# Performance work log

Measured on AMD Instinct MI355X. Metric: run time of the kernel, lower is better.

The kernel has to match this reference:

```python
import jax, jax.numpy as jnp
import numpy as np

B, S, C, L = 8, 256, 4, 256
E, H, NL, NS = 256, 8, 2, 8
DH = E // H
EPS = 1e-5


def _conv1d(x, w, b):
    # x: [B, Cin, L], w: [Cout, Cin, K] -> [B, Cout, L] (SAME padding, stride 1)
    y = jax.lax.conv_general_dilated(x, w, (1,), 'SAME', dimension_numbers=('NCH', 'OIH', 'NCH'))
    return y + b[None, :, None]


def _local_cnn(xs, w1, b1, w2, b2):
    # xs: [B, 4, L] for one segment; per-segment weights
    h = jax.nn.relu(_conv1d(xs, w1, b1))
    h = jax.nn.relu(_conv1d(h, w2, b2))
    return jnp.max(h, axis=-1)  # AdaptiveMaxPool1d(1) + squeeze -> [B, E]


def _layernorm(x, g, b):
    m = jnp.mean(x, axis=-1, keepdims=True)
    v = jnp.mean((x - m) ** 2, axis=-1, keepdims=True)
    return (x - m) / jnp.sqrt(v + EPS) * g + b


def setup_inputs() -> dict:
    key = jax.random.key(0)
    ks = jax.random.split(key, 24)
    n = lambda k, shp, s: jax.random.normal(k, shp, jnp.float32) * s
    return {
        'x': jax.random.normal(ks[0], (B, S, C, L), jnp.float32),
        'conv1_w': n(ks[1], (S, 128, 4, 3), 0.1), 'conv1_b': jnp.zeros((S, 128), jnp.float32),
        'conv2_w': n(ks[2], (S, E, 128, 3), 0.05), 'conv2_b': jnp.zeros((S, E), jnp.float32),
        'ln1_g': jnp.ones((NL, E), jnp.float32), 'ln1_b': jnp.zeros((NL, E), jnp.float32),
        'wq': n(ks[3], (NL, E, E), 0.02), 'bq': jnp.zeros((NL, E), jnp.float32),
        'wk': n(ks[4], (NL, E, E), 0.02), 'bk': jnp.zeros((NL, E), jnp.float32),
        'wv': n(ks[5], (NL, E, E), 0.02), 'bv': jnp.zeros((NL, E), jnp.float32),
        'wo': n(ks[6], (NL, E, E), 0.02), 'bo': jnp.zeros((NL, E), jnp.float32),
        'bias_w': n(ks[7], (NL, 4, H), 0.1), 'bias_b': jnp.zeros((NL, H), jnp.float32),
        'ln2_g': jnp.ones((NL, E), jnp.float32), 'ln2_b': jnp.zeros((NL, E), jnp.float32),
        'ffn_w1': n(ks[8], (NL, E, 2 * E), 0.02), 'ffn_b1': jnp.zeros((NL, 2 * E), jnp.float32),
        'ffn_w2': n(ks[9], (NL, 2 * E, E), 0.02), 'ffn_b2': jnp.zeros((NL, E), jnp.float32),
        'fc_w': n(ks[10], (NS * E, 2), 0.02), 'fc_b': jnp.zeros((2,), jnp.float32),
    }


def _forward(x, conv1_w, conv1_b, conv2_w, conv2_b, ln1_g, ln1_b,
             wq, bq, wk, bk, wv, bv, wo, bo, bias_w, bias_b,
             ln2_g, ln2_b, ffn_w1, ffn_b1, ffn_w2, ffn_b2, fc_w, fc_b):
    # Per-segment CNNs (vmap over segment axis with per-segment weights) -> [B, S, E]
    cnn = jax.vmap(_local_cnn, in_axes=(1, 0, 0, 0, 0), out_axes=1)(x, conv1_w, conv1_b, conv2_w, conv2_b)
    feat = _layernorm(cnn, jnp.ones((E,), cnn.dtype), jnp.zeros((E,), cnn.dtype))  # F.layer_norm, no affine

    # bias matrices: cdist (p=2), global-max normalized; positional distance; inverses
    sq = jnp.sum(feat * feat, axis=-1)  # [B, S]
    d2 = sq[:, :, None] + sq[:, None, :] - 2.0 * jnp.einsum('bie,bje->bij', feat, feat)
    dist = jnp.sqrt(jnp.maximum(d2, 0.0))
    dist = dist / (jnp.max(dist) + 1e-6)
    idx = jnp.arange(S, dtype=feat.dtype)
    rdist = jnp.abs(idx[:, None] - idx[None, :]) / (S - 1)
    rdist = jnp.broadcast_to(rdist[None], (feat.shape[0], S, S))
    attn_bias = jnp.stack([dist, rdist, 1.0 - rdist, 1.0 - dist], axis=-1)  # [B,S,S,4]

    h = feat
    scale = 1.0 / jnp.sqrt(jnp.asarray(DH, h.dtype))
    for l in range(NL):
        hn = _layernorm(h, ln1_g[l], ln1_b[l])
        q = (hn @ wq[l] + bq[l]).reshape(-1, S, H, DH)
        k = (hn @ wk[l] + bk[l]).reshape(-1, S, H, DH)
        v = (hn @ wv[l] + bv[l]).reshape(-1, S, H, DH)
        scores = jnp.einsum('bihd,bjhd->bhij', q, k) * scale
        scores = scores + jnp.einsum('bijc,ch->bhij', attn_bias, bias_w[l]) + bias_b[l][None, :, None, None]
        a = jax.nn.softmax(scores, axis=-1)
        o = jnp.einsum('bhij,bjhd->bihd', a, v).reshape(-1, S, E) @ wo[l] + bo[l]
        h = h + o
        hn2 = _layernorm(h, ln2_g[l], ln2_b[l])
        f = jax.nn.relu(hn2 @ ffn_w1[l] + ffn_b1[l]) @ ffn_w2[l] + ffn_b2[l]
        h = h + f

    # split into NS chunks along segments, max-pool each, concat (S % NS == 0)
    pooled = jnp.max(h.reshape(-1, NS, S // NS, E), axis=2).reshape(-1, NS * E)
    return pooled @ fc_w + fc_b  # [B, num_classes]


def reference(x, conv1_w, conv1_b, conv2_w, conv2_b, ln1_g, ln1_b,
              wq, bq, wk, bk, wv, bv, wo, bo, bias_w, bias_b,
              ln2_g, ln2_b, ffn_w1, ffn_b1, ffn_w2, ffn_b2, fc_w, fc_b):
    return _forward(x, conv1_w, conv1_b, conv2_w, conv2_b, ln1_g, ln1_b,
                    wq, bq, wk, bk, wv, bv, wo, bo, bias_w, bias_b,
                    ln2_g, ln2_b, ffn_w1, ffn_b1, ffn_w2, ffn_b2, fc_w, fc_b)
```

## Files before the change

kernel.cpp:

```cpp
#include <hip/hip_runtime.h>
#include <hip/hip_bf16.h>


typedef float floatx4 __attribute__((ext_vector_type(4)));
typedef short bf16x8 __attribute__((ext_vector_type(8)));

__device__ __forceinline__ float wave_sum(float v) {
    v += __shfl_xor(v, 32); v += __shfl_xor(v, 16); v += __shfl_xor(v, 8);
    v += __shfl_xor(v, 4);  v += __shfl_xor(v, 2);  v += __shfl_xor(v, 1);
    return v;
}
__device__ __forceinline__ float wave_max(float v) {
    v = fmaxf(v, __shfl_xor(v, 32)); v = fmaxf(v, __shfl_xor(v, 16));
    v = fmaxf(v, __shfl_xor(v, 8));  v = fmaxf(v, __shfl_xor(v, 4));
    v = fmaxf(v, __shfl_xor(v, 2));  v = fmaxf(v, __shfl_xor(v, 1));
    return v;
}
__device__ __forceinline__ unsigned short f2bf(float v) {
    unsigned b = __float_as_uint(v);
    unsigned r = (b + 0x7fffu + ((b >> 16) & 1u)) >> 16;
    return (unsigned short)r;
}

__global__ void init_kernel(unsigned* dmax, unsigned* cnnmax) {
    const size_t i = (size_t)blockIdx.x * 256 + threadIdx.x;
    cnnmax[i] = 0u;
    if (i == 0) *dmax = 0u;
}

__global__ __launch_bounds__(256) void prep_w2_kernel(
    const float* __restrict__ w2, unsigned short* __restrict__ w2b)
{
    const int s = blockIdx.x;
    const int part = blockIdx.y;
    const float* src = w2 + (size_t)s * 98304;
    unsigned short* dst = w2b + (size_t)s * 98304;
    for (int o = part * 24576 + threadIdx.x; o < (part + 1) * 24576; o += 256) {
        const int kk = o % 384, co = o / 384;
        const int ci = kk & 127, tap = kk >> 7;
        dst[o] = f2bf(src[(size_t)co * 384 + ci * 3 + tap]);
    }
}

__global__ __launch_bounds__(512) void conv2_fused_kernel(
    const unsigned short* __restrict__ w2b,
    const float* __restrict__ x,
    const float* __restrict__ w1,
    const float* __restrict__ b1,
    const float* __restrict__ b2,
    unsigned* __restrict__ cnnmax)
{
    __shared__ float xs[4][258];
    __shared__ float w1s[1536];
    __shared__ unsigned short Hs[130 * 136];
    const int tid = threadIdx.x;
    const int lane = tid & 63;
    const int wv = __builtin_amdgcn_readfirstlane((int)(tid >> 6));
    const int wm = wv & 3, wn = wv >> 2;
    const int s = blockIdx.x;
    const int nt = blockIdx.y;
    const int b = nt >> 1;
    const int l0 = (nt & 1) * 128;
    const int lr = lane & 15;
    const int quad = lane >> 4;
    const int qk = quad * 8;

    const float* xp = x + ((size_t)(b * 256 + s)) * 1024;
    for (int i = tid; i < 1024; i += 512) {
        const int ci = i >> 8, l = i & 255;
        xs[ci][l + 1] = xp[i];
    }
    if (tid < 4) { xs[tid][0] = 0.f; xs[tid][257] = 0.f; }
    const float* w1p = w1 + (size_t)s * 1536;
    for (int i = tid; i < 1536; i += 512) w1s[i] = w1p[i];
    __syncthreads();

    {
        const int co = tid & 127;
        const int g = tid >> 7;
        float wreg[12];
#pragma unroll
        for (int k = 0; k < 12; k++) wreg[k] = w1s[co * 12 + k];
        const float bb1 = b1[s * 128 + co];
        for (int pr = g; pr < 130; pr += 4) {
            const int l = l0 - 1 + pr;
            float a = 0.f;
            if ((unsigned)l < 256u) {
                a = bb1;
#pragma unroll
                for (int ci = 0; ci < 4; ci++)
#pragma unroll
                    for (int k = 0; k < 3; k++) a = fmaf(wreg[ci * 3 + k], xs[ci][l + k], a);
                a = fmaxf(a, 0.f);
            }
            Hs[pr * 136 + co] = f2bf(a);
        }
    }
    __syncthreads();

    floatx4 acc[4][4];
#pragma unroll
    for (int r = 0; r < 4; r++)
#pragma unroll
        for (int c = 0; c < 4; c++) acc[r][c] = (floatx4){0.f, 0.f, 0.f, 0.f};

    const int co_base = wm * 64;
    const unsigned short* wp = w2b + ((size_t)(s * 256 + co_base + lr)) * 384 + qk;
    const int nb = wn * 64;

#pragma unroll
    for (int tap = 0; tap < 3; tap++) {
#pragma unroll
        for (int ci0 = 0; ci0 < 128; ci0 += 32) {
            const int kk0 = tap * 128 + ci0;
            bf16x8 a[4], bb[4];
#pragma unroll
            for (int r = 0; r < 4; r++)
                a[r] = *(const bf16x8*)(wp + r * (16 * 384) + kk0);
#pragma unroll
            for (int c = 0; c < 4; c++) {
                const int rl = nb + c * 16 + lr + tap;
                bb[c] = *(const bf16x8*)(&Hs[rl * 136 + ci0 + qk]);
            }
#pragma unroll
            for (int r = 0; r < 4; r++)
#pragma unroll
                for (int c = 0; c < 4; c++)
                    acc[r][c] = __builtin_amdgcn_mfma_f32_16x16x32_bf16(a[r], bb[c], acc[r][c], 0, 0, 0);
        }
    }

    const float* b2s = b2 + s * 256;
    unsigned* cmrow = cnnmax + ((size_t)(b * 256 + s)) * 256;
#pragma unroll
    for (int r = 0; r < 4; r++) {
#pragma unroll
        for (int e = 0; e < 4; e++) {
            const int co = co_base + r * 16 + quad * 4 + e;
            const float bias = b2s[co];
            float mv = 0.f;
#pragma unroll
            for (int c = 0; c < 4; c++) mv = fmaxf(mv, acc[r][c][e] + bias);
            mv = fmaxf(mv, __shfl_xor(mv, 1));
            mv = fmaxf(mv, __shfl_xor(mv, 2));
            mv = fmaxf(mv, __shfl_xor(mv, 4));
            mv = fmaxf(mv, __shfl_xor(mv, 8));
            if (lr == 0) atomicMax(&cmrow[co], __float_as_uint(mv));
        }
    }
}

__global__ __launch_bounds__(256) void ln0_kernel(
    const unsigned* __restrict__ cm, float* __restrict__ out, float* __restrict__ sqv)
{
    const int tid = threadIdx.x, lane = tid & 63, wid = tid >> 6;
    const int row = blockIdx.x * 4 + wid;
    const unsigned* xr = cm + (size_t)row * 256;
    float v[4];
#pragma unroll
    for (int i = 0; i < 4; i++) v[i] = __uint_as_float(xr[lane + 64 * i]);
    float sm = wave_sum(v[0] + v[1] + v[2] + v[3]);
    const float mean = sm * (1.f / 256.f);
    float qv = 0.f;
#pragma unroll
    for (int i = 0; i < 4; i++) { const float d = v[i] - mean; qv = fmaf(d, d, qv); }
    qv = wave_sum(qv);
    const float inv = rsqrtf(qv * (1.f / 256.f) + 1e-5f);
    float* orow = out + (size_t)row * 256;
#pragma unroll
    for (int i = 0; i < 4; i++) orow[lane + 64 * i] = (v[i] - mean) * inv;
    if (lane == 0) sqv[row] = qv * inv * inv;
}

__global__ __launch_bounds__(256) void dist_kernel(
    const float* __restrict__ feat, const float* __restrict__ sq,
    float* __restrict__ dist, unsigned* __restrict__ dmax)
{
    __shared__ float Fi[32][260];
    __shared__ float Fj[16][260];
    __shared__ float redm[4];
    const int tid = threadIdx.x;
    const int bid = blockIdx.x;
    const int b = bid >> 7, it = (bid >> 4) & 7, jt = bid & 15;
    const float* fb = feat + (size_t)b * 65536;
    for (int idx = tid; idx < 32 * 256; idx += 256) {
        const int r = idx >> 8, e = idx & 255;
        Fi[r][e] = fb[(it * 32 + r) * 256 + e];
    }
    for (int idx = tid; idx < 16 * 256; idx += 256) {
        const int r = idx >> 8, e = idx & 255;
        Fj[r][e] = fb[(jt * 16 + r) * 256 + e];
    }
    __syncthreads();
    const int ii = tid >> 3, j0 = (tid & 7) * 2;
    float acc[2] = {0.f, 0.f};
    for (int e = 0; e < 256; e += 4) {
        const float4 a = *(const float4*)&Fi[ii][e];
#pragma unroll
        for (int u = 0; u < 2; u++) {
            const float4 bv = *(const float4*)&Fj[j0 + u][e];
            acc[u] += a.x * bv.x + a.y * bv.y + a.z * bv.z + a.w * bv.w;
        }
    }
    const float sqi = sq[b * 256 + it * 32 + ii];
    float mymax = 0.f;
#pragma unroll
    for (int u = 0; u < 2; u++) {
        const float d2 = sqi + sq[b * 256 + jt * 16 + j0 + u] - 2.f * acc[u];
        const float d = sqrtf(fmaxf(d2, 0.f));
        dist[((size_t)b * 256 + it * 32 + ii) * 256 + jt * 16 + j0 + u] = d;
        mymax = fmaxf(mymax, d);
    }
    mymax = wave_max(mymax);
    if ((tid & 63) == 0) redm[tid >> 6] = mymax;
    __syncthreads();
    if (tid == 0) {
        const float m = fmaxf(fmaxf(redm[0], redm[1]), fmaxf(redm[2], redm[3]));
        atomicMax(dmax, __float_as_uint(m));
    }
}

__global__ __launch_bounds__(256) void ln_bf_kernel(
    const float* __restrict__ x, const float* __restrict__ g, const float* __restrict__ bta,
    unsigned short* __restrict__ out)
{
    const int tid = threadIdx.x, lane = tid & 63, wid = tid >> 6;
    const int row = blockIdx.x * 4 + wid;
    const float* xr = x + (size_t)row * 256;
    float v[4];
#pragma unroll
    for (int i = 0; i < 4; i++) v[i] = xr[lane + 64 * i];
    float sm = wave_sum(v[0] + v[1] + v[2] + v[3]);
    const float mean = sm * (1.f / 256.f);
    float q = 0.f;
#pragma unroll
    for (int i = 0; i < 4; i++) { const float d = v[i] - mean; q = fmaf(d, d, q); }
    q = wave_sum(q);
    const float inv = rsqrtf(q * (1.f / 256.f) + 1e-5f);
    unsigned short* orow = out + (size_t)row * 256;
#pragma unroll
    for (int i = 0; i < 4; i++) {
        const int e = lane + 64 * i;
        orow[e] = f2bf((v[i] - mean) * inv * g[e] + bta[e]);
    }
}

__global__ __launch_bounds__(256) void prep_wt_kernel(
    const float* __restrict__ wq, const float* __restrict__ wk, const float* __restrict__ wv,
    const float* __restrict__ wo, const float* __restrict__ f1, const float* __restrict__ f2,
    unsigned short* __restrict__ wtb)
{
    __shared__ float t[32][33];
    const int z = blockIdx.z;
    const int l = z / 6, id = z % 6;
    const float* src; int K_, N_; size_t doff;
    switch (id) {
        case 0:  src = wq + (size_t)l * 65536;  K_ = 256; N_ = 256; doff = 0;      break;
        case 1:  src = wk + (size_t)l * 65536;  K_ = 256; N_ = 256; doff = 65536;  break;
        case 2:  src = wv + (size_t)l * 65536;  K_ = 256; N_ = 256; doff = 131072; break;
        case 3:  src = wo + (size_t)l * 65536;  K_ = 256; N_ = 256; doff = 196608; break;
        case 4:  src = f1 + (size_t)l * 131072; K_ = 256; N_ = 512; doff = 262144; break;
        default: src = f2 + (size_t)l * 131072; K_ = 512; N_ = 256; doff = 393216; break;
    }
    const int k0 = blockIdx.x * 32, n0 = blockIdx.y * 32;
    if (k0 >= K_ || n0 >= N_) return;
    unsigned short* dst = wtb + (size_t)l * 524288 + doff;
    const int c = threadIdx.x & 31, rq = threadIdx.x >> 5;
#pragma unroll
    for (int i = 0; i < 4; i++) {
        const int r = rq + i * 8;
        t[r][c] = src[(size_t)(k0 + r) * N_ + n0 + c];
    }
    __syncthreads();
#pragma unroll
    for (int i = 0; i < 4; i++) {
        const int r = rq + i * 8;
        dst[(size_t)(n0 + r) * K_ + k0 + c] = f2bf(t[c][r]);
    }
}

__global__ __launch_bounds__(128) void gemm_mfma_kernel(
    const unsigned short* __restrict__ A, const unsigned short* __restrict__ Wt,
    const float* __restrict__ b0, const float* __restrict__ b1, const float* __restrict__ b2,
    const float* __restrict__ R, float* __restrict__ outf,
    unsigned short* __restrict__ o0, unsigned short* __restrict__ o1, unsigned short* __restrict__ o2,
    int K, int mode)
{
    const int tid = threadIdx.x;
    const int lane = tid & 63, lr = lane & 15, quad = lane >> 4;
    const int wv = __builtin_amdgcn_readfirstlane((int)(tid >> 6));
    const int m0 = blockIdx.x * 128 + wv * 64;
    const int n0 = blockIdx.y * 32;

    floatx4 acc[4][2];
#pragma unroll
    for (int r = 0; r < 4; r++)
#pragma unroll
        for (int c = 0; c < 2; c++) acc[r][c] = (floatx4){0.f, 0.f, 0.f, 0.f};

    const unsigned short* Ap = A + (size_t)(m0 + lr) * K + quad * 8;
    const unsigned short* Bp = Wt + (size_t)(n0 + lr) * K + quad * 8;
    const int nks = K >> 5;
#pragma unroll 4
    for (int ks = 0; ks < nks; ks++) {
        const int ko = ks * 32;
        bf16x8 a[4], b[2];
#pragma unroll
        for (int r = 0; r < 4; r++) a[r] = *(const bf16x8*)(Ap + (size_t)r * 16 * K + ko);
#pragma unroll
        for (int c = 0; c < 2; c++) b[c] = *(const bf16x8*)(Bp + (size_t)c * 16 * K + ko);
#pragma unroll
        for (int r = 0; r < 4; r++)
#pragma unroll
            for (int c = 0; c < 2; c++)
                acc[r][c] = __builtin_amdgcn_mfma_f32_16x16x32_bf16(a[r], b[c], acc[r][c], 0, 0, 0);
    }

    if (mode == 0) {
        const int which = n0 >> 8, nn0 = n0 & 255;
        if (which < 2) {
            unsigned short* op = which ? o1 : o0;
            const float* bp = which ? b1 : b0;
#pragma unroll
            for (int r = 0; r < 4; r++)
#pragma unroll
                for (int c = 0; c < 2; c++)
#pragma unroll
                    for (int e = 0; e < 4; e++) {
                        const int m = m0 + r * 16 + quad * 4 + e;
                        const int n = nn0 + c * 16 + lr;
                        op[(size_t)m * 256 + n] = f2bf(acc[r][c][e] + bp[n]);
                    }
        } else {
#pragma unroll
            for (int r = 0; r < 4; r++)
#pragma unroll
                for (int c = 0; c < 2; c++)
#pragma unroll
                    for (int e = 0; e < 4; e++) {
                        const int m = m0 + r * 16 + quad * 4 + e;
                        const int nn = nn0 + c * 16 + lr;
                        const int bb_ = m >> 8, j = m & 255, hh = nn >> 5, d = nn & 31;
                        o2[(size_t)((bb_ * 8 + hh) * 32 + d) * 256 + j] = f2bf(acc[r][c][e] + b2[nn]);
                    }
        }
    } else if (mode == 1) {
#pragma unroll
        for (int r = 0; r < 4; r++)
#pragma unroll
            for (int c = 0; c < 2; c++)
#pragma unroll
                for (int e = 0; e < 4; e++) {
                    const int m = m0 + r * 16 + quad * 4 + e;
                    const int n = n0 + c * 16 + lr;
                    outf[(size_t)m * 256 + n] = acc[r][c][e] + b0[n] + R[(size_t)m * 256 + n];
                }
    } else {
#pragma unroll
        for (int r = 0; r < 4; r++)
#pragma unroll
            for (int c = 0; c < 2; c++)
#pragma unroll
                for (int e = 0; e < 4; e++) {
                    const int m = m0 + r * 16 + quad * 4 + e;
                    const int n = n0 + c * 16 + lr;
                    o0[(size_t)m * 512 + n] = f2bf(fmaxf(acc[r][c][e] + b0[n], 0.f));
                }
    }
}

__global__ __launch_bounds__(256) void attn_mfma_kernel(
    const unsigned short* __restrict__ q_bf, const unsigned short* __restrict__ k_bf,
    const unsigned short* __restrict__ vt_bf,
    const float* __restrict__ dist, const unsigned* __restrict__ dmax,
    const float* __restrict__ bw, const float* __restrict__ bb,
    unsigned short* __restrict__ ao_bf)
{
    __shared__ unsigned short Ps[4][16][264];
    const int tid = threadIdx.x;
    const int lane = tid & 63, lr = lane & 15, quad = lane >> 4;
    const int wv = __builtin_amdgcn_readfirstlane((int)(tid >> 6));
    const int ic = blockIdx.x, hh = blockIdx.y, b = blockIdx.z;
    const int i0 = ic * 64 + wv * 16;

    const float dinv = 1.f / (__uint_as_float(*dmax) + 1e-6f);
    const float w0 = bw[0 * 8 + hh], w1 = bw[1 * 8 + hh], w2 = bw[2 * 8 + hh], w3 = bw[3 * 8 + hh];
    const float bbh = bb[hh];
    const float scale = 0.17677669529663687f;

    const bf16x8 aq = *(const bf16x8*)(q_bf + (size_t)(b * 256 + i0 + lr) * 256 + hh * 32 + quad * 8);
    floatx4 sc[16];
#pragma unroll
    for (int c = 0; c < 16; c++) {
        const bf16x8 bk = *(const bf16x8*)(k_bf + (size_t)(b * 256 + c * 16 + lr) * 256 + hh * 32 + quad * 8);
        sc[c] = __builtin_amdgcn_mfma_f32_16x16x32_bf16(aq, bk, (floatx4){0.f, 0.f, 0.f, 0.f}, 0, 0, 0);
    }

#pragma unroll
    for (int e = 0; e < 4; e++) {
        const int i = i0 + quad * 4 + e;
        const float* drow = dist + ((size_t)(b * 256 + i)) * 256;
        float bs[16];
        float mx = -1e30f;
#pragma unroll
        for (int c = 0; c < 16; c++) {
            const int j = c * 16 + lr;
            const float dn = drow[j] * dinv;
            const float rd = fabsf((float)(i - j)) * (1.f / 255.f);
            bs[c] = sc[c][e] * scale + w0 * dn + w1 * rd + w2 * (1.f - rd) + w3 * (1.f - dn) + bbh;
            mx = fmaxf(mx, bs[c]);
        }
        mx = fmaxf(mx, __shfl_xor(mx, 1)); mx = fmaxf(mx, __shfl_xor(mx, 2));
        mx = fmaxf(mx, __shfl_xor(mx, 4)); mx = fmaxf(mx, __shfl_xor(mx, 8));
        float sm = 0.f;
#pragma unroll
        for (int c = 0; c < 16; c++) { bs[c] = __expf(bs[c] - mx); sm += bs[c]; }
        sm += __shfl_xor(sm, 1); sm += __shfl_xor(sm, 2);
        sm += __shfl_xor(sm, 4); sm += __shfl_xor(sm, 8);
        const float rs = 1.f / sm;
#pragma unroll
        for (int c = 0; c < 16; c++)
            Ps[wv][quad * 4 + e][c * 16 + lr] = f2bf(bs[c] * rs);
    }
    __syncthreads();

    floatx4 oc[2];
    oc[0] = (floatx4){0.f, 0.f, 0.f, 0.f};
    oc[1] = (floatx4){0.f, 0.f, 0.f, 0.f};
    const unsigned short* vtb = vt_bf + (size_t)(b * 8 + hh) * 8192;
#pragma unroll
    for (int ks = 0; ks < 8; ks++) {
        const bf16x8 ap = *(const bf16x8*)(&Ps[wv][lr][ks * 32 + quad * 8]);
#pragma unroll
        for (int c2 = 0; c2 < 2; c2++) {
            const bf16x8 bvv = *(const bf16x8*)(vtb + (size_t)(c2 * 16 + lr) * 256 + ks * 32 + quad * 8);
            oc[c2] = __builtin_amdgcn_mfma_f32_16x16x32_bf16(ap, bvv, oc[c2], 0, 0, 0);
        }
    }
#pragma unroll
    for (int c2 = 0; c2 < 2; c2++)
#pragma unroll
        for (int e = 0; e < 4; e++)
            ao_bf[(size_t)(b * 256 + i0 + quad * 4 + e) * 256 + hh * 32 + c2 * 16 + lr] = f2bf(oc[c2][e]);
}

__global__ __launch_bounds__(256) void pool_fc_kernel(
    const float* __restrict__ h, const float* __restrict__ fcw,
    const float* __restrict__ fcb, float* __restrict__ out)
{
    __shared__ float red[8];
    const int b = blockIdx.x, tid = threadIdx.x, lane = tid & 63, wid = tid >> 6;
    float a0 = 0.f, a1 = 0.f;
    for (int ns = 0; ns < 8; ns++) {
        const float* hp = h + ((size_t)(b * 256 + ns * 32)) * 256 + tid;
        float m = hp[0];
#pragma unroll
        for (int r = 1; r < 32; r++) m = fmaxf(m, hp[(size_t)r * 256]);
        a0 = fmaf(m, fcw[(ns * 256 + tid) * 2 + 0], a0);
        a1 = fmaf(m, fcw[(ns * 256 + tid) * 2 + 1], a1);
    }
    a0 = wave_sum(a0);
    a1 = wave_sum(a1);
    if (lane == 0) { red[wid] = a0; red[4 + wid] = a1; }
    __syncthreads();
    if (tid == 0) out[b * 2 + 0] = red[0] + red[1] + red[2] + red[3] + fcb[0];
    if (tid == 1) out[b * 2 + 1] = red[4] + red[5] + red[6] + red[7] + fcb[1];
}

extern "C" void kernel_launch(void* const* d_in, const int* in_sizes, int n_in,
                              void* d_out, int out_size, void* d_ws, size_t ws_size,
                              hipStream_t stream)
{
    (void)in_sizes; (void)n_in; (void)out_size; (void)ws_size;
    const float* x       = (const float*)d_in[0];
    const float* conv1_w = (const float*)d_in[1];
    const float* conv1_b = (const float*)d_in[2];
    const float* conv2_w = (const float*)d_in[3];
    const float* conv2_b = (const float*)d_in[4];
    const float* ln1_g   = (const float*)d_in[5];
    const float* ln1_b   = (const float*)d_in[6];
    const float* wq = (const float*)d_in[7];  const float* bq = (const float*)d_in[8];
    const float* wk = (const float*)d_in[9];  const float* bk = (const float*)d_in[10];
    const float* wvp = (const float*)d_in[11]; const float* bv = (const float*)d_in[12];
    const float* wo = (const float*)d_in[13]; const float* bo = (const float*)d_in[14];
    const float* bias_w = (const float*)d_in[15];
    const float* bias_b = (const float*)d_in[16];
    const float* ln2_g  = (const float*)d_in[17];
    const float* ln2_b  = (const float*)d_in[18];
    const float* ffn_w1 = (const float*)d_in[19]; const float* ffn_b1 = (const float*)d_in[20];
    const float* ffn_w2 = (const float*)d_in[21]; const float* ffn_b2 = (const float*)d_in[22];
    const float* fc_w   = (const float*)d_in[23]; const float* fc_b = (const float*)d_in[24];
    float* out = (float*)d_out;

    float* ws = (float*)d_ws;
    float* h    = ws;
    float* dist = h + 524288;
    float* sqv  = dist + 524288;
    unsigned* dmax = (unsigned*)(sqv + 2048);
    unsigned* cnnmax = (unsigned*)(sqv + 2048 + 16);
    unsigned short* hn_bf = (unsigned short*)(sqv + 2048 + 16 + 524288);
    unsigned short* q_bf  = hn_bf + 524288;
    unsigned short* k_bf  = q_bf + 524288;
    unsigned short* vt_bf = k_bf + 524288;
    unsigned short* ao_bf = vt_bf + 524288;
    unsigned short* fm_bf = ao_bf + 524288;
    unsigned short* wtb   = fm_bf + 1048576;
    unsigned short* w2b   = wtb + 1048576;

    init_kernel<<<2048, 256, 0, stream>>>(dmax, cnnmax);
    prep_wt_kernel<<<dim3(16, 16, 12), 256, 0, stream>>>(wq, wk, wvp, wo, ffn_w1, ffn_w2, wtb);
    prep_w2_kernel<<<dim3(256, 4), 256, 0, stream>>>(conv2_w, w2b);
    conv2_fused_kernel<<<dim3(256, 16), 512, 0, stream>>>(
        w2b, x, conv1_w, conv1_b, conv2_b, cnnmax);
    ln0_kernel<<<512, 256, 0, stream>>>(cnnmax, h, sqv);
    dist_kernel<<<1024, 256, 0, stream>>>(h, sqv, dist, dmax);

    for (int l = 0; l < 2; l++) {
        const unsigned short* wqkvT = wtb + (size_t)l * 524288;
        const unsigned short* woT   = wqkvT + 196608;
        const unsigned short* f1T   = wqkvT + 262144;
        const unsigned short* f2T   = wqkvT + 393216;

        ln_bf_kernel<<<512, 256, 0, stream>>>(h, ln1_g + l * 256, ln1_b + l * 256, hn_bf);
        gemm_mfma_kernel<<<dim3(16, 24), 128, 0, stream>>>(
            hn_bf, wqkvT, bq + l * 256, bk + l * 256, bv + l * 256,
            nullptr, nullptr, q_bf, k_bf, vt_bf, 256, 0);
        attn_mfma_kernel<<<dim3(4, 8, 8), 256, 0, stream>>>(
            q_bf, k_bf, vt_bf, dist, dmax, bias_w + l * 32, bias_b + l * 8, ao_bf);
        gemm_mfma_kernel<<<dim3(16, 8), 128, 0, stream>>>(
            ao_bf, woT, bo + l * 256, nullptr, nullptr,
            h, h, nullptr, nullptr, nullptr, 256, 1);
        ln_bf_kernel<<<512, 256, 0, stream>>>(h, ln2_g + l * 256, ln2_b + l * 256, hn_bf);
        gemm_mfma_kernel<<<dim3(16, 16), 128, 0, stream>>>(
            hn_bf, f1T, ffn_b1 + l * 512, nullptr, nullptr,
            nullptr, nullptr, fm_bf, nullptr, nullptr, 256, 2);
        gemm_mfma_kernel<<<dim3(16, 8), 128, 0, stream>>>(
            fm_bf, f2T, ffn_b2 + l * 256, nullptr, nullptr,
            h, h, nullptr, nullptr, nullptr, 512, 1);
    }
    pool_fc_kernel<<<8, 256, 0, stream>>>(h, fc_w, fc_b, out);
}
```

Baseline: 611.7 us.

## Double-buffer conv2 weight chunks into LDS via async global_load_lds with swizzle

The fused conv2 kernel used to read bf16 weight fragments directly from global memory inside the MFMA loop. Now the weight prep writes a swizzled chunked layout, and each K-step's 256x32 weight chunk is staged into a double-buffered LDS area with asynchronous global_load_lds. This overlaps the next chunk's load with the current MFMAs and with the conv1 prologue, and the swizzle avoids LDS bank conflicts. In exchange it adds 32 KB of LDS, two barriers per step and a min-blocks launch bound, which may lower occupancy.

```diff
diff --git a/kernel.cpp b/kernel.cpp
--- a/kernel.cpp
+++ b/kernel.cpp
@@ -22,6 +22,21 @@
     return (unsigned short)r;
 }
 
+typedef const __attribute__((address_space(1))) unsigned int* gas_u32p;
+typedef __attribute__((address_space(3))) unsigned int* las_u32p;
+
+__device__ __forceinline__ void stage_chunk(const unsigned short* gbase,
+                                            unsigned short* lbase,
+                                            int wv, int lane)
+{
+    const char* g = (const char*)gbase + (wv << 11) + (lane << 4);
+    char* l = (char*)lbase + (wv << 11);
+    __builtin_amdgcn_global_load_lds((gas_u32p)(const void*)g,
+                                     (las_u32p)(void*)l, 16, 0, 0);
+    __builtin_amdgcn_global_load_lds((gas_u32p)(const void*)(g + 1024),
+                                     (las_u32p)(void*)(l + 1024), 16, 0, 0);
+}
+
 __global__ void init_kernel(unsigned* dmax, unsigned* cnnmax) {
     const size_t i = (size_t)blockIdx.x * 256 + threadIdx.x;
     cnnmax[i] = 0u;
@@ -36,13 +51,19 @@
     const float* src = w2 + (size_t)s * 98304;
     unsigned short* dst = w2b + (size_t)s * 98304;
     for (int o = part * 24576 + threadIdx.x; o < (part + 1) * 24576; o += 256) {
-        const int kk = o % 384, co = o / 384;
+        const int c  = o >> 13;
+        const int w  = o & 8191;
+        const int co = w >> 5;
+        const int up = (w >> 3) & 3;
+        const int t  = w & 7;
+        const int u  = (up ^ co ^ (co >> 2)) & 3;
+        const int kk = c * 32 + u * 8 + t;
         const int ci = kk & 127, tap = kk >> 7;
         dst[o] = f2bf(src[(size_t)co * 384 + ci * 3 + tap]);
     }
 }
 
-__global__ __launch_bounds__(512) void conv2_fused_kernel(
+__global__ __launch_bounds__(512, 4) void conv2_fused_kernel(
     const unsigned short* __restrict__ w2b,
     const float* __restrict__ x,
     const float* __restrict__ w1,
@@ -53,6 +74,8 @@
     __shared__ float xs[4][258];
     __shared__ float w1s[1536];
     __shared__ unsigned short Hs[130 * 136];
+    __shared__ unsigned short Ab[2][8192];
+
     const int tid = threadIdx.x;
     const int lane = tid & 63;
     const int wv = __builtin_amdgcn_readfirstlane((int)(tid >> 6));
@@ -73,15 +96,19 @@
     if (tid < 4) { xs[tid][0] = 0.f; xs[tid][257] = 0.f; }
     const float* w1p = w1 + (size_t)s * 1536;
     for (int i = tid; i < 1536; i += 512) w1s[i] = w1p[i];
+    const int co1 = tid & 127;
+    const float bb1 = b1[s * 128 + co1];
     __syncthreads();
 
+    const unsigned short* wchunks = w2b + (size_t)s * 98304;
+    stage_chunk(wchunks,        &Ab[0][0], wv, lane);
+    stage_chunk(wchunks + 8192, &Ab[1][0], wv, lane);
+
     {
-        const int co = tid & 127;
         const int g = tid >> 7;
         float wreg[12];
 #pragma unroll
-        for (int k = 0; k < 12; k++) wreg[k] = w1s[co * 12 + k];
-        const float bb1 = b1[s * 128 + co];
+        for (int k = 0; k < 12; k++) wreg[k] = w1s[co1 * 12 + k];
         for (int pr = g; pr < 130; pr += 4) {
             const int l = l0 - 1 + pr;
             float a = 0.f;
@@ -93,10 +120,11 @@
                     for (int k = 0; k < 3; k++) a = fmaf(wreg[ci * 3 + k], xs[ci][l + k], a);
                 a = fmaxf(a, 0.f);
             }
-            Hs[pr * 136 + co] = f2bf(a);
+            Hs[pr * 136 + co1] = f2bf(a);
         }
     }
-    __syncthreads();
+    asm volatile("s_waitcnt lgkmcnt(0)" ::: "memory");
+    __builtin_amdgcn_s_barrier();
 
     floatx4 acc[4][4];
 #pragma unroll
@@ -104,31 +132,44 @@
 #pragma unroll
         for (int c = 0; c < 4; c++) acc[r][c] = (floatx4){0.f, 0.f, 0.f, 0.f};
 
-    const int co_base = wm * 64;
-    const unsigned short* wp = w2b + ((size_t)(s * 256 + co_base + lr)) * 384 + qk;
     const int nb = wn * 64;
-
-#pragma unroll
-    for (int tap = 0; tap < 3; tap++) {
-#pragma unroll
-        for (int ci0 = 0; ci0 < 128; ci0 += 32) {
-            const int kk0 = tap * 128 + ci0;
-            bf16x8 a[4], bb[4];
-#pragma unroll
-            for (int r = 0; r < 4; r++)
-                a[r] = *(const bf16x8*)(wp + r * (16 * 384) + kk0);
-#pragma unroll
-            for (int c = 0; c < 4; c++) {
-                const int rl = nb + c * 16 + lr + tap;
-                bb[c] = *(const bf16x8*)(&Hs[rl * 136 + ci0 + qk]);
-            }
-#pragma unroll
-            for (int r = 0; r < 4; r++)
-#pragma unroll
-                for (int c = 0; c < 4; c++)
-                    acc[r][c] = __builtin_amdgcn_mfma_f32_16x16x32_bf16(a[r], bb[c], acc[r][c], 0, 0, 0);
-        }
-    }
+    const int aoff = wm * 2048 + lr * 32 + (((quad ^ lr ^ (lr >> 2)) & 3) * 8);
+    const int hbase = (nb + lr) * 136 + qk;
+
+#define CSTEP(KS, BUF, WAITN, DOSTAGE)                                          \
+    {                                                                            \
+        asm volatile("s_waitcnt vmcnt(" #WAITN ")" ::: "memory");                \
+        __builtin_amdgcn_s_barrier();                                            \
+        __builtin_amdgcn_sched_barrier(0);                                       \
+        const int tap_ = (KS) >> 2, ci0_ = ((KS) & 3) * 32;                      \
+        const unsigned short* ap = &Ab[BUF][aoff];                               \
+        const unsigned short* hp = &Hs[hbase + tap_ * 136 + ci0_];               \
+        bf16x8 a[4], bb[4];                                                      \
+        _Pragma("unroll")                                                        \
+        for (int r = 0; r < 4; r++) a[r] = *(const bf16x8*)(ap + r * 512);       \
+        _Pragma("unroll")                                                        \
+        for (int c = 0; c < 4; c++) bb[c] = *(const bf16x8*)(hp + c * 2176);     \
+        _Pragma("unroll")                                                        \
+        for (int r = 0; r < 4; r++)                                              \
+            _Pragma("unroll")                                                    \
+            for (int c = 0; c < 4; c++)                                          \
+                acc[r][c] = __builtin_amdgcn_mfma_f32_16x16x32_bf16(             \
+                    a[r], bb[c], acc[r][c], 0, 0, 0);                            \
+        __builtin_amdgcn_sched_barrier(0);                                       \
+        __builtin_amdgcn_s_barrier();                                            \
+        __builtin_amdgcn_sched_barrier(0);                                       \
+        if (DOSTAGE)                                                             \
+            stage_chunk(wchunks + ((KS) + 2) * 8192, &Ab[BUF][0], wv, lane);     \
+    }
+
+    for (int kp = 0; kp < 5; kp++) {
+        const int ks = kp * 2;
+        CSTEP(ks,     0, 2, 1);
+        CSTEP(ks + 1, 1, 2, 1);
+    }
+    CSTEP(10, 0, 2, 0);
+    CSTEP(11, 1, 0, 0);
+#undef CSTEP
 
     const float* b2s = b2 + s * 256;
     unsigned* cmrow = cnnmax + ((size_t)(b * 256 + s)) * 256;
@@ -136,7 +177,7 @@
     for (int r = 0; r < 4; r++) {
 #pragma unroll
         for (int e = 0; e < 4; e++) {
-            const int co = co_base + r * 16 + quad * 4 + e;
+            const int co = wm * 64 + r * 16 + quad * 4 + e;
             const float bias = b2s[co];
             float mv = 0.f;
 #pragma unroll
```

Measured after the change: 576.8 us. -5.7%, faster.
